# Performance work log

Measured on AMD Instinct MI355X. Metric: run time of the kernel, lower is better.

## Reference

```python
import jax, jax.numpy as jnp
import numpy as np

N_EDGES = 1_600_000
N_NODES = 100_000
D_FEAT = 64


def setup_inputs() -> dict:
    key = jax.random.key(0)
    k1, k2 = jax.random.split(key)
    messages = jax.random.normal(k1, (N_EDGES, D_FEAT), dtype=jnp.float32)
    dst = jax.random.randint(k2, (N_EDGES,), 0, N_NODES, dtype=jnp.int64)
    return {"messages": messages, "dst": dst, "num_nodes": N_NODES}


def reference(messages, dst, num_nodes):
    # aggregators = ['sum', 'mean', 'max', 'std'] (module default)
    N = num_nodes
    ones = jnp.ones((dst.shape[0],), dtype=messages.dtype)
    # sum aggregation
    s = jax.ops.segment_sum(messages, dst, num_segments=N)  # [N, D]
    # degree, clamped to >= 1 (as in scatter_count)
    deg = jnp.maximum(jax.ops.segment_sum(ones, dst, num_segments=N), 1.0)[:, None]  # [N, 1]
    # mean aggregation
    mean = s / deg
    # max aggregation; empty segments yield -inf -> replaced with 0
    mx = jax.ops.segment_max(messages, dst, num_segments=N)
    mx = jnp.where(jnp.isfinite(mx), mx, jnp.zeros((), dtype=messages.dtype))
    # std aggregation: mean of squared deviations from per-node mean
    sq_diff = (messages - mean[dst]) ** 2
    var = jax.ops.segment_sum(sq_diff, dst, num_segments=N) / deg
    std = jnp.sqrt(var + 1e-8)
    return jnp.concatenate([s, mean, mx, std], axis=-1)  # [N, 4*D]
```

## Files before the change

kernel.cpp:

```cpp
#include <hip/hip_runtime.h>
#include <float.h>


#define BLK 256

__global__ void zero_counts(int* __restrict__ counts, int N) {
    int i = blockIdx.x * BLK + threadIdx.x;
    if (i < N) counts[i] = 0;
}

__global__ void hist_rank(const int* __restrict__ dst, int stride,
                          int* __restrict__ counts, int* __restrict__ rank, int E) {
    int e = blockIdx.x * BLK + threadIdx.x;
    if (e < E) {
        int n = (stride == 2) ? (int)((const long long*)dst)[e] : dst[e];
        rank[e] = atomicAdd(&counts[n], 1);
    }
}

__global__ void scatter_rank(const int* __restrict__ dst, int stride,
                             const int* __restrict__ lofs, const int* __restrict__ partials,
                             const int* __restrict__ rank, int* __restrict__ perm, int E) {
    int e = blockIdx.x * BLK + threadIdx.x;
    if (e < E) {
        int n = (stride == 2) ? (int)((const long long*)dst)[e] : dst[e];
        perm[lofs[n] + partials[n >> 8] + rank[e]] = e;
    }
}

__global__ void scan1(const int* __restrict__ counts, int* __restrict__ lofs,
                      int* __restrict__ partials, int N) {
    __shared__ int s[BLK];
    int t = threadIdx.x;
    int i = blockIdx.x * BLK + t;
    int x = (i < N) ? counts[i] : 0;
    s[t] = x;
    __syncthreads();
    for (int o = 1; o < BLK; o <<= 1) {
        int y = (t >= o) ? s[t - o] : 0;
        __syncthreads();
        s[t] += y;
        __syncthreads();
    }
    if (i < N) lofs[i] = s[t] - x;
    if (t == BLK - 1) partials[blockIdx.x] = s[t];
}

__global__ void scan2(int* __restrict__ partials, int NB) {
    __shared__ int s[512];
    int t = threadIdx.x;
    int x = (t < NB) ? partials[t] : 0;
    s[t] = x;
    __syncthreads();
    for (int o = 1; o < 512; o <<= 1) {
        int y = (t >= o) ? s[t - o] : 0;
        __syncthreads();
        s[t] += y;
        __syncthreads();
    }
    if (t < NB) partials[t] = s[t] - x;
}

__global__ void hist(const int* __restrict__ dst, int stride, int* __restrict__ counts, int E) {
    int e = blockIdx.x * BLK + threadIdx.x;
    if (e < E) {
        int n = (stride == 2) ? (int)((const long long*)dst)[e] : dst[e];
        atomicAdd(&counts[n], 1);
    }
}

__global__ void cursor_init(const int* __restrict__ lofs, const int* __restrict__ partials,
                            int* __restrict__ cursor, int N) {
    int i = blockIdx.x * BLK + threadIdx.x;
    if (i < N) cursor[i] = lofs[i] + partials[i >> 8];
}

__global__ void permscatter(const int* __restrict__ dst, int stride,
                            int* __restrict__ cursor, int* __restrict__ perm, int E) {
    int e = blockIdx.x * BLK + threadIdx.x;
    if (e < E) {
        int n = (stride == 2) ? (int)((const long long*)dst)[e] : dst[e];
        int pos = atomicAdd(&cursor[n], 1);
        perm[pos] = e;
    }
}

__global__ void reduce(const float* __restrict__ msg, const int* __restrict__ perm,
                       const int* __restrict__ lofs, const int* __restrict__ partials,
                       const int* __restrict__ counts, float* __restrict__ out, int N) {
    int node = blockIdx.x * 4 + (threadIdx.x >> 6);
    if (node >= N) return;
    int lane = threadIdx.x & 63;
    int beg = lofs[node] + partials[node >> 8];
    int deg_i = counts[node];
    int end = beg + deg_i;

    float s0 = 0.f, s1 = 0.f, s2 = 0.f, s3 = 0.f;
    float q0 = 0.f, q1 = 0.f, q2 = 0.f, q3 = 0.f;
    float m0 = -FLT_MAX, m1 = -FLT_MAX, m2 = -FLT_MAX, m3 = -FLT_MAX;

    const float* mp = msg + lane;

    for (int base = beg; base < end; base += 64) {
        int cnt = end - base;
        if (cnt > 64) cnt = 64;
        int idx = base + lane;
        if (idx >= end) idx = end - 1;
        int eid_l = perm[idx];

        int j = 0;
        for (; j + 8 <= cnt; j += 8) {
            int e0 = __shfl(eid_l, j + 0);
            int e1 = __shfl(eid_l, j + 1);
            int e2 = __shfl(eid_l, j + 2);
            int e3 = __shfl(eid_l, j + 3);
            int e4 = __shfl(eid_l, j + 4);
            int e5 = __shfl(eid_l, j + 5);
            int e6 = __shfl(eid_l, j + 6);
            int e7 = __shfl(eid_l, j + 7);
            float v0 = mp[(long long)e0 << 6];
            float v1 = mp[(long long)e1 << 6];
            float v2 = mp[(long long)e2 << 6];
            float v3 = mp[(long long)e3 << 6];
            float v4 = mp[(long long)e4 << 6];
            float v5 = mp[(long long)e5 << 6];
            float v6 = mp[(long long)e6 << 6];
            float v7 = mp[(long long)e7 << 6];
            s0 += v0; q0 += v0 * v0; m0 = fmaxf(m0, v0);
            s1 += v1; q1 += v1 * v1; m1 = fmaxf(m1, v1);
            s2 += v2; q2 += v2 * v2; m2 = fmaxf(m2, v2);
            s3 += v3; q3 += v3 * v3; m3 = fmaxf(m3, v3);
            s0 += v4; q0 += v4 * v4; m0 = fmaxf(m0, v4);
            s1 += v5; q1 += v5 * v5; m1 = fmaxf(m1, v5);
            s2 += v6; q2 += v6 * v6; m2 = fmaxf(m2, v6);
            s3 += v7; q3 += v7 * v7; m3 = fmaxf(m3, v7);
        }
        for (; j + 4 <= cnt; j += 4) {
            int e0 = __shfl(eid_l, j + 0);
            int e1 = __shfl(eid_l, j + 1);
            int e2 = __shfl(eid_l, j + 2);
            int e3 = __shfl(eid_l, j + 3);
            float v0 = mp[(long long)e0 << 6];
            float v1 = mp[(long long)e1 << 6];
            float v2 = mp[(long long)e2 << 6];
            float v3 = mp[(long long)e3 << 6];
            s0 += v0; q0 += v0 * v0; m0 = fmaxf(m0, v0);
            s1 += v1; q1 += v1 * v1; m1 = fmaxf(m1, v1);
            s2 += v2; q2 += v2 * v2; m2 = fmaxf(m2, v2);
            s3 += v3; q3 += v3 * v3; m3 = fmaxf(m3, v3);
        }
        for (; j < cnt; ++j) {
            int e = __shfl(eid_l, j);
            float v = mp[(long long)e << 6];
            s0 += v; q0 += v * v; m0 = fmaxf(m0, v);
        }
    }

    float s  = (s0 + s1) + (s2 + s3);
    float sq = (q0 + q1) + (q2 + q3);
    float mx = fmaxf(fmaxf(m0, m1), fmaxf(m2, m3));

    float deg  = fmaxf((float)deg_i, 1.0f);
    float mean = s / deg;
    float var  = fmaxf(sq / deg - mean * mean, 0.0f);
    float mxo  = (deg_i > 0) ? mx : 0.0f;

    float* base_out = out + (long long)node * 256;
    base_out[lane]       = s;
    base_out[64 + lane]  = mean;
    base_out[128 + lane] = mxo;
    base_out[192 + lane] = sqrtf(var + 1e-8f);
}

extern "C" void kernel_launch(void* const* d_in, const int* in_sizes, int n_in,
                              void* d_out, int out_size, void* d_ws, size_t ws_size,
                              hipStream_t stream) {
    const float* msg = (const float*)d_in[0];
    const int*   dst = (const int*)d_in[1];
    float* out = (float*)d_out;

    int E = in_sizes[0] / 64;
    int N = out_size / 256;
    int stride = (in_sizes[1] == 2 * E) ? 2 : 1;

    int* counts   = (int*)d_ws;
    int* lofs     = counts + N;
    int* partials = lofs + N;
    int* perm     = partials + 512;
    int* extra    = perm + E;

    int NB_N = (N + BLK - 1) / BLK;
    int NB_E = (E + BLK - 1) / BLK;

    size_t need_rank = ((size_t)2 * N + 512 + (size_t)2 * E) * sizeof(int);

    zero_counts<<<NB_N, BLK, 0, stream>>>(counts, N);

    if (ws_size >= need_rank) {
        int* rank = extra;
        hist_rank<<<NB_E, BLK, 0, stream>>>(dst, stride, counts, rank, E);
        scan1<<<NB_N, BLK, 0, stream>>>(counts, lofs, partials, N);
        scan2<<<1, 512, 0, stream>>>(partials, NB_N);
        scatter_rank<<<NB_E, BLK, 0, stream>>>(dst, stride, lofs, partials, rank, perm, E);
    } else {
        int* cursor = extra;
        hist<<<NB_E, BLK, 0, stream>>>(dst, stride, counts, E);
        scan1<<<NB_N, BLK, 0, stream>>>(counts, lofs, partials, N);
        scan2<<<1, 512, 0, stream>>>(partials, NB_N);
        cursor_init<<<NB_N, BLK, 0, stream>>>(lofs, partials, cursor, N);
        permscatter<<<NB_E, BLK, 0, stream>>>(dst, stride, cursor, perm, E);
    }

    reduce<<<(N + 3) / 4, BLK, 0, stream>>>(msg, perm, lofs, partials, counts, out, N);
}
```

Measured before the change: 664.3 us.

## Vectorize gather-reduce with float4 rows and pair-process edges in sort kernels

The reduce kernel now has each wavefront load float4 chunks, with 16 lanes covering one 64-float row and four edges fetched per load instruction. Partial sums, squared sums and maxes are combined across the four lane groups with xor shuffles, and the results are written with float4 nontemporal stores. The aim is fewer, wider memory instructions on the irregular gather. hist_rank and scatter_rank now handle two edges per thread with vectorized index and rank loads. The costs are extra cross-lane reductions, more idle lanes on the tail of low-degree nodes, and a changed floating-point summation order.

```diff
diff --git a/kernel.cpp b/kernel.cpp
--- a/kernel.cpp
+++ b/kernel.cpp
@@ -3,6 +3,15 @@
 
 
 #define BLK 256
+
+typedef float v4f __attribute__((ext_vector_type(4)));
+
+__device__ __forceinline__ v4f fmax4(v4f a, v4f b) {
+    v4f r;
+    r.x = fmaxf(a.x, b.x); r.y = fmaxf(a.y, b.y);
+    r.z = fmaxf(a.z, b.z); r.w = fmaxf(a.w, b.w);
+    return r;
+}
 
 __global__ void zero_counts(int* __restrict__ counts, int N) {
     int i = blockIdx.x * BLK + threadIdx.x;
@@ -11,8 +20,18 @@
 
 __global__ void hist_rank(const int* __restrict__ dst, int stride,
                           int* __restrict__ counts, int* __restrict__ rank, int E) {
-    int e = blockIdx.x * BLK + threadIdx.x;
-    if (e < E) {
+    int p = blockIdx.x * BLK + threadIdx.x;
+    int npair = E >> 1;
+    if (p < npair) {
+        int n0, n1;
+        if (stride == 2) { int4 v = ((const int4*)dst)[p]; n0 = v.x; n1 = v.z; }
+        else             { int2 v = ((const int2*)dst)[p]; n0 = v.x; n1 = v.y; }
+        int r0 = atomicAdd(&counts[n0], 1);
+        int r1 = atomicAdd(&counts[n1], 1);
+        *(int2*)(rank + 2 * p) = make_int2(r0, r1);
+    }
+    if ((E & 1) && p == npair) {
+        int e = E - 1;
         int n = (stride == 2) ? (int)((const long long*)dst)[e] : dst[e];
         rank[e] = atomicAdd(&counts[n], 1);
     }
@@ -21,8 +40,18 @@
 __global__ void scatter_rank(const int* __restrict__ dst, int stride,
                              const int* __restrict__ lofs, const int* __restrict__ partials,
                              const int* __restrict__ rank, int* __restrict__ perm, int E) {
-    int e = blockIdx.x * BLK + threadIdx.x;
-    if (e < E) {
+    int p = blockIdx.x * BLK + threadIdx.x;
+    int npair = E >> 1;
+    if (p < npair) {
+        int n0, n1;
+        if (stride == 2) { int4 v = ((const int4*)dst)[p]; n0 = v.x; n1 = v.z; }
+        else             { int2 v = ((const int2*)dst)[p]; n0 = v.x; n1 = v.y; }
+        int2 r = *(const int2*)(rank + 2 * p);
+        perm[lofs[n0] + partials[n0 >> 8] + r.x] = 2 * p;
+        perm[lofs[n1] + partials[n1 >> 8] + r.y] = 2 * p + 1;
+    }
+    if ((E & 1) && p == npair) {
+        int e = E - 1;
         int n = (stride == 2) ? (int)((const long long*)dst)[e] : dst[e];
         perm[lofs[n] + partials[n >> 8] + rank[e]] = e;
     }
@@ -91,15 +120,18 @@
     int node = blockIdx.x * 4 + (threadIdx.x >> 6);
     if (node >= N) return;
     int lane = threadIdx.x & 63;
-    int beg = lofs[node] + partials[node >> 8];
+    int qid  = lane >> 4;
+    int fq   = lane & 15;
+
+    int beg   = lofs[node] + partials[node >> 8];
     int deg_i = counts[node];
-    int end = beg + deg_i;
-
-    float s0 = 0.f, s1 = 0.f, s2 = 0.f, s3 = 0.f;
-    float q0 = 0.f, q1 = 0.f, q2 = 0.f, q3 = 0.f;
-    float m0 = -FLT_MAX, m1 = -FLT_MAX, m2 = -FLT_MAX, m3 = -FLT_MAX;
-
-    const float* mp = msg + lane;
+    int end   = beg + deg_i;
+
+    v4f s4 = {0.f, 0.f, 0.f, 0.f};
+    v4f q4 = {0.f, 0.f, 0.f, 0.f};
+    v4f m4 = {-FLT_MAX, -FLT_MAX, -FLT_MAX, -FLT_MAX};
+
+    const v4f* __restrict__ msg4 = (const v4f*)msg;
 
     for (int base = beg; base < end; base += 64) {
         int cnt = end - base;
@@ -110,66 +142,58 @@
 
         int j = 0;
         for (; j + 8 <= cnt; j += 8) {
-            int e0 = __shfl(eid_l, j + 0);
-            int e1 = __shfl(eid_l, j + 1);
-            int e2 = __shfl(eid_l, j + 2);
-            int e3 = __shfl(eid_l, j + 3);
-            int e4 = __shfl(eid_l, j + 4);
-            int e5 = __shfl(eid_l, j + 5);
-            int e6 = __shfl(eid_l, j + 6);
-            int e7 = __shfl(eid_l, j + 7);
-            float v0 = mp[(long long)e0 << 6];
-            float v1 = mp[(long long)e1 << 6];
-            float v2 = mp[(long long)e2 << 6];
-            float v3 = mp[(long long)e3 << 6];
-            float v4 = mp[(long long)e4 << 6];
-            float v5 = mp[(long long)e5 << 6];
-            float v6 = mp[(long long)e6 << 6];
-            float v7 = mp[(long long)e7 << 6];
-            s0 += v0; q0 += v0 * v0; m0 = fmaxf(m0, v0);
-            s1 += v1; q1 += v1 * v1; m1 = fmaxf(m1, v1);
-            s2 += v2; q2 += v2 * v2; m2 = fmaxf(m2, v2);
-            s3 += v3; q3 += v3 * v3; m3 = fmaxf(m3, v3);
-            s0 += v4; q0 += v4 * v4; m0 = fmaxf(m0, v4);
-            s1 += v5; q1 += v5 * v5; m1 = fmaxf(m1, v5);
-            s2 += v6; q2 += v6 * v6; m2 = fmaxf(m2, v6);
-            s3 += v7; q3 += v7 * v7; m3 = fmaxf(m3, v7);
+            int ea = __shfl(eid_l, j + qid);
+            int eb = __shfl(eid_l, j + 4 + qid);
+            v4f va = __builtin_nontemporal_load(msg4 + (((long long)ea << 4) + fq));
+            v4f vb = __builtin_nontemporal_load(msg4 + (((long long)eb << 4) + fq));
+            s4 += va; q4 += va * va; m4 = fmax4(m4, va);
+            s4 += vb; q4 += vb * vb; m4 = fmax4(m4, vb);
         }
-        for (; j + 4 <= cnt; j += 4) {
-            int e0 = __shfl(eid_l, j + 0);
-            int e1 = __shfl(eid_l, j + 1);
-            int e2 = __shfl(eid_l, j + 2);
-            int e3 = __shfl(eid_l, j + 3);
-            float v0 = mp[(long long)e0 << 6];
-            float v1 = mp[(long long)e1 << 6];
-            float v2 = mp[(long long)e2 << 6];
-            float v3 = mp[(long long)e3 << 6];
-            s0 += v0; q0 += v0 * v0; m0 = fmaxf(m0, v0);
-            s1 += v1; q1 += v1 * v1; m1 = fmaxf(m1, v1);
-            s2 += v2; q2 += v2 * v2; m2 = fmaxf(m2, v2);
-            s3 += v3; q3 += v3 * v3; m3 = fmaxf(m3, v3);
+        int rem = cnt - j;
+        if (rem > 0) {
+            int sa = j + qid;
+            int ea = __shfl(eid_l, (sa < cnt) ? sa : (cnt - 1));
+            v4f va = __builtin_nontemporal_load(msg4 + (((long long)ea << 4) + fq));
+            if (sa < cnt) { s4 += va; q4 += va * va; m4 = fmax4(m4, va); }
+            if (rem > 4) {
+                int sb = j + 4 + qid;
+                int eb = __shfl(eid_l, (sb < cnt) ? sb : (cnt - 1));
+                v4f vb = __builtin_nontemporal_load(msg4 + (((long long)eb << 4) + fq));
+                if (sb < cnt) { s4 += vb; q4 += vb * vb; m4 = fmax4(m4, vb); }
+            }
         }
-        for (; j < cnt; ++j) {
-            int e = __shfl(eid_l, j);
-            float v = mp[(long long)e << 6];
-            s0 += v; q0 += v * v; m0 = fmaxf(m0, v);
-        }
-    }
-
-    float s  = (s0 + s1) + (s2 + s3);
-    float sq = (q0 + q1) + (q2 + q3);
-    float mx = fmaxf(fmaxf(m0, m1), fmaxf(m2, m3));
-
-    float deg  = fmaxf((float)deg_i, 1.0f);
-    float mean = s / deg;
-    float var  = fmaxf(sq / deg - mean * mean, 0.0f);
-    float mxo  = (deg_i > 0) ? mx : 0.0f;
-
-    float* base_out = out + (long long)node * 256;
-    base_out[lane]       = s;
-    base_out[64 + lane]  = mean;
-    base_out[128 + lane] = mxo;
-    base_out[192 + lane] = sqrtf(var + 1e-8f);
+    }
+
+    #pragma unroll
+    for (int off = 16; off <= 32; off <<= 1) {
+        s4.x += __shfl_xor(s4.x, off); s4.y += __shfl_xor(s4.y, off);
+        s4.z += __shfl_xor(s4.z, off); s4.w += __shfl_xor(s4.w, off);
+        q4.x += __shfl_xor(q4.x, off); q4.y += __shfl_xor(q4.y, off);
+        q4.z += __shfl_xor(q4.z, off); q4.w += __shfl_xor(q4.w, off);
+        m4.x = fmaxf(m4.x, __shfl_xor(m4.x, off));
+        m4.y = fmaxf(m4.y, __shfl_xor(m4.y, off));
+        m4.z = fmaxf(m4.z, __shfl_xor(m4.z, off));
+        m4.w = fmaxf(m4.w, __shfl_xor(m4.w, off));
+    }
+
+    if (qid == 0) {
+        float deg = fmaxf((float)deg_i, 1.0f);
+        v4f mean = s4 / deg;
+        v4f var  = q4 / deg - mean * mean;
+        var.x = fmaxf(var.x, 0.f); var.y = fmaxf(var.y, 0.f);
+        var.z = fmaxf(var.z, 0.f); var.w = fmaxf(var.w, 0.f);
+        v4f stdv;
+        stdv.x = sqrtf(var.x + 1e-8f); stdv.y = sqrtf(var.y + 1e-8f);
+        stdv.z = sqrtf(var.z + 1e-8f); stdv.w = sqrtf(var.w + 1e-8f);
+        v4f mx = m4;
+        if (deg_i == 0) { mx.x = 0.f; mx.y = 0.f; mx.z = 0.f; mx.w = 0.f; }
+
+        v4f* bo = (v4f*)(out + (long long)node * 256);
+        __builtin_nontemporal_store(s4,   bo + fq);
+        __builtin_nontemporal_store(mean, bo + 16 + fq);
+        __builtin_nontemporal_store(mx,   bo + 32 + fq);
+        __builtin_nontemporal_store(stdv, bo + 48 + fq);
+    }
 }
 
 extern "C" void kernel_launch(void* const* d_in, const int* in_sizes, int n_in,
@@ -191,6 +215,8 @@
 
     int NB_N = (N + BLK - 1) / BLK;
     int NB_E = (E + BLK - 1) / BLK;
+    int NT_P = ((E + 1) >> 1);
+    int NB_P = (NT_P + BLK - 1) / BLK;
 
     size_t need_rank = ((size_t)2 * N + 512 + (size_t)2 * E) * sizeof(int);
 
@@ -198,10 +224,10 @@
 
     if (ws_size >= need_rank) {
         int* rank = extra;
-        hist_rank<<<NB_E, BLK, 0, stream>>>(dst, stride, counts, rank, E);
+        hist_rank<<<NB_P, BLK, 0, stream>>>(dst, stride, counts, rank, E);
         scan1<<<NB_N, BLK, 0, stream>>>(counts, lofs, partials, N);
         scan2<<<1, 512, 0, stream>>>(partials, NB_N);
-        scatter_rank<<<NB_E, BLK, 0, stream>>>(dst, stride, lofs, partials, rank, perm, E);
+        scatter_rank<<<NB_P, BLK, 0, stream>>>(dst, stride, lofs, partials, rank, perm, E);
     } else {
         int* cursor = extra;
         hist<<<NB_E, BLK, 0, stream>>>(dst, stride, counts, E);
```

After: 642.2 us. 1.03x faster.
